# Performance work log

Measured on AMD Instinct MI355X. Metric: run time of the kernel, lower is better.

## Reference

```python
import jax, jax.numpy as jnp
import numpy as np

T, B = 512, 64
IDIM, HDIM = 256, 512
NSTACK, SSZ, SDIM, SDEPTH = 2, 32, 64, 2
NACTS = 3  # push, pop, noop


def setup_inputs() -> dict:
    key = jax.random.key(0)
    ks = jax.random.split(key, 16)
    s = 0.02
    inp = {
        "embs": jax.random.normal(ks[0], (T, B, IDIM), jnp.float32),
        "lens": jax.random.randint(ks[1], (B,), 1, T + 1),
        # emb2hid
        "We": jax.random.normal(ks[2], (HDIM, IDIM), jnp.float32) * s,
        "be": jnp.zeros((HDIM,), jnp.float32),
        # hid2hid
        "Wh": jax.random.normal(ks[3], (HDIM, HDIM), jnp.float32) * s,
        "bh": jnp.zeros((HDIM,), jnp.float32),
        # hid2act
        "Wa": jax.random.normal(ks[4], (NSTACK * NACTS, HDIM), jnp.float32) * s,
        "ba": jnp.zeros((NSTACK * NACTS,), jnp.float32),
        # hid2stack
        "Ws": jax.random.normal(ks[5], (NSTACK * SDIM, HDIM), jnp.float32) * s,
        "bs": jnp.zeros((NSTACK * SDIM,), jnp.float32),
        # stack2hid
        "Wr": jax.random.normal(ks[6], (NSTACK * HDIM, NSTACK * SDIM * SDEPTH), jnp.float32) * s,
        "br": jnp.zeros((NSTACK * HDIM,), jnp.float32),
        # non-trainable stack init bias
        "mem_bias": jax.random.uniform(ks[7], (NSTACK, SDIM), jnp.float32,
                                        -1.0, 1.0) / np.sqrt(NSTACK * SSZ + SDIM),
    }
    return inp


def reference(embs, lens, We, be, Wh, bh, Wa, ba, Ws, bs, Wr, br, mem_bias):
    Tn, Bn, _ = embs.shape
    mem = jnp.broadcast_to(mem_bias[None, :, None, :], (Bn, NSTACK, 1, SDIM))
    stack0 = jnp.broadcast_to(mem_bias[None, :, None, :], (Bn, NSTACK, SSZ, SDIM))
    hid0 = jnp.zeros((Bn, HDIM), embs.dtype)
    res0 = jnp.zeros_like(stack0)

    def step(carry, xs):
        hid, stack, res = carry
        emb, t = xs
        mhid = emb @ We.T + be + hid @ Wh.T + bh
        # read top sdepth cells of each stack
        tops = stack[:, :, :SDEPTH, :].reshape(Bn, -1)
        read = (tops @ Wr.T + br).reshape(Bn, NSTACK, HDIM).sum(axis=1)
        mhid = mhid + read
        # action gating (push/pop/noop) per stack
        act = jax.nn.softmax((hid @ Wa.T + ba).reshape(Bn, NSTACK, NACTS), axis=-1)
        p_push = act[..., 0, None, None]  # [B, nstack, 1, 1]
        p_pop = act[..., 1, None, None]
        p_noop = act[..., 2, None, None]
        push_vals = jnp.tanh((hid @ Ws.T + bs).reshape(Bn, NSTACK, SDIM))
        # push: shift down, write push_vals on top; pop: shift up, mem_bias at bottom
        stack_push = jnp.concatenate([push_vals[:, :, None, :], stack[:, :, :-1, :]], axis=2)
        stack_pop = jnp.concatenate([stack[:, :, 1:, :], mem], axis=2)
        new_stack = p_push * stack_push + p_pop * stack_pop + p_noop * stack
        new_hid = jnp.tanh(mhid)
        new_res = jnp.where((t == lens - 1)[:, None, None, None], new_stack, res)
        return (new_hid, new_stack, new_res), new_hid

    (_, _, stack_res), output = jax.lax.scan(
        step, (hid0, stack0, res0), (embs, jnp.arange(Tn)))
    hid_last = output[lens - 1, jnp.arange(Bn), :][None]  # [1, B, H]
    return output, hid_last, stack_res
```

## Files before the change

### kernel.cpp

```cpp
#include <hip/hip_runtime.h>
#include <hip/hip_bf16.h>
#include <hip/hip_fp16.h>
#include <stdint.h>

constexpr int kT = 512;

constexpr uint32_t WHP_OFF  = 0u;
constexpr uint32_t WRSP_OFF = 524288u;
constexpr uint32_t WSP_OFF  = 786432u;
constexpr uint32_t WEP_OFF  = 917504u;
constexpr uint32_t BIAS_OFF = 1179648u;
constexpr uint32_t X_OFF    = 1181696u;

constexpr uint32_t OUT_HL = 16777216u;
constexpr uint32_t OUT_SR = 16809984u;

static __device__ __forceinline__ float bitsf(uint32_t u) {
  union { uint32_t u; float f; } c; c.u = u; return c.f;
}

typedef _Float16 h2_t __attribute__((ext_vector_type(2)));

static __device__ __forceinline__ float dot2acc(uint32_t w, uint32_t h, float acc) {
#if __has_builtin(__builtin_amdgcn_fdot2)
  return __builtin_amdgcn_fdot2(__builtin_bit_cast(h2_t, w),
                                __builtin_bit_cast(h2_t, h), acc, false);
#else
  h2_t wv = __builtin_bit_cast(h2_t, w), hv = __builtin_bit_cast(h2_t, h);
  return acc + (float)wv.x * (float)hv.x + (float)wv.y * (float)hv.y;
#endif
}

static __device__ __forceinline__ float dot8h(uint4 w, uint4 h, float acc) {
  acc = dot2acc(w.x, h.x, acc);
  acc = dot2acc(w.y, h.y, acc);
  acc = dot2acc(w.z, h.z, acc);
  acc = dot2acc(w.w, h.w, acc);
  return acc;
}

__global__ __launch_bounds__(256) void pack_kernel(
    const float* __restrict__ Wh, const float* __restrict__ Wr,
    const float* __restrict__ Ws, const float* __restrict__ We,
    const float* __restrict__ be, const float* __restrict__ bh,
    const float* __restrict__ br, char* __restrict__ ws)
{
  uint32_t g = blockIdx.x * 256u + threadIdx.x;
  __half* whp  = (__half*)(ws + WHP_OFF);
  __half* wrsp = (__half*)(ws + WRSP_OFF);
  __half* wsp  = (__half*)(ws + WSP_OFF);
  __hip_bfloat16* wep = (__hip_bfloat16*)(ws + WEP_OFF);
  float* bias = (float*)(ws + BIAS_OFF);

  if (g < 262144u) {
    uint32_t e = g & 7u, h = (g >> 3) & 511u, kb = g >> 12;
    whp[g] = __float2half(Wh[h * 512u + kb * 8u + e]);
  }
  if (g < 131072u) {
    uint32_t e = g & 7u, h = (g >> 3) & 511u, jb = g >> 12;
    wrsp[g] = __float2half(Wr[h * 256u + jb * 8u + e] +
                           Wr[(512u + h) * 256u + jb * 8u + e]);
  }
  if (g < 65536u) {
    uint32_t e = g & 7u, o = (g >> 3) & 127u, kb = g >> 10;
    wsp[g] = __float2half(Ws[o * 512u + kb * 8u + e]);
  }
  if (g < 131072u) {
    uint32_t e = g & 7u, h = (g >> 3) & 511u, kb = g >> 12;
    wep[g] = __float2bfloat16(We[h * 256u + kb * 8u + e]);
  }
  if (g < 512u) bias[g] = be[g] + bh[g] + br[g] + br[512u + g];
}

__global__ __launch_bounds__(256) void embed_kernel(
    const float* __restrict__ embs, const char* __restrict__ ws,
    float* __restrict__ out)
{
  __shared__ __align__(16) float embL[16 * 256];
  const uint32_t tid = threadIdx.x;
  const uint32_t r0 = blockIdx.x * 16u;
  #pragma unroll
  for (int i = 0; i < 16; i++) embL[tid + i * 256] = embs[r0 * 256u + tid + i * 256u];
  __syncthreads();

  const uint4* wep = (const uint4*)(ws + WEP_OFF);
  const float* bias = (const float*)(ws + BIAS_OFF);

  for (int hb = 0; hb < 2; hb++) {
    uint32_t h = hb * 256u + tid;
    float acc[16];
    #pragma unroll
    for (int r = 0; r < 16; r++) acc[r] = 0.f;
    for (int kb = 0; kb < 32; kb++) {
      uint4 v = wep[kb * 512u + h];
      float w0 = bitsf(v.x << 16), w1 = bitsf(v.x & 0xffff0000u);
      float w2 = bitsf(v.y << 16), w3 = bitsf(v.y & 0xffff0000u);
      float w4 = bitsf(v.z << 16), w5 = bitsf(v.z & 0xffff0000u);
      float w6 = bitsf(v.w << 16), w7 = bitsf(v.w & 0xffff0000u);
      #pragma unroll
      for (int r = 0; r < 16; r++) {
        const float4* e4 = (const float4*)&embL[r * 256 + kb * 8];
        float4 a = e4[0], c = e4[1];
        acc[r] += w0 * a.x + w1 * a.y + w2 * a.z + w3 * a.w
                + w4 * c.x + w5 * c.y + w6 * c.z + w7 * c.w;
      }
    }
    float bi = bias[h];
    #pragma unroll
    for (int r = 0; r < 16; r++) out[(r0 + r) * 512u + h] = acc[r] + bi;
  }
}

__global__ __launch_bounds__(1024) void rnn_kernel(
    const int* __restrict__ lens, const float* __restrict__ Wa,
    const float* __restrict__ ba, const float* __restrict__ bs,
    const float* __restrict__ memb, char* __restrict__ ws,
    float* __restrict__ out)
{
  __shared__ __align__(16) float stk[2][4096];
  __shared__ __align__(16) __half waH[3072];
  __shared__ __align__(16) __half hH[2][512];
  __shared__ __align__(16) __half tH[2][256];
  __shared__ __align__(16) float pvL[128];
  __shared__ __align__(16) float membL[128];
  __shared__ float bsL[128];
  __shared__ float lgts[8];
  __shared__ float baL[8];

  const uint32_t tid = threadIdx.x;
  const uint32_t wg = blockIdx.x;
  const uint32_t q = wg >> 6;
  const uint32_t b = wg & 63u;
  const int len = lens[b];
  const uint32_t r = tid >> 3, s = tid & 7u;
  const uint32_t h = q * 128u + r;

  const uint4* whp  = (const uint4*)(ws + WHP_OFF);
  const uint4* wrsp = (const uint4*)(ws + WRSP_OFF);
  const uint4* wsp  = (const uint4*)(ws + WSP_OFF);
  uint32_t* X32 = (uint32_t*)(ws + X_OFF);

  uint4 wh[8], wrs[4], wsr[8];
  #pragma unroll
  for (int i = 0; i < 8; i++) wh[i]  = whp[(s * 8u + (uint32_t)i) * 512u + h];
  #pragma unroll
  for (int i = 0; i < 4; i++) wrs[i] = wrsp[(s * 4u + (uint32_t)i) * 512u + h];
  #pragma unroll
  for (int j = 0; j < 8; j++) wsr[j] = wsp[(s * 8u + (uint32_t)j) * 128u + r];

  for (uint32_t i = tid; i < 3072u; i += 1024u) waH[i] = __float2half(Wa[i]);
  if (tid < 128u) { membL[tid] = memb[tid]; bsL[tid] = bs[tid]; }
  if (tid < 64u)  ((uint4*)hH[0])[tid] = uint4{0u, 0u, 0u, 0u};
  if (tid < 256u) {
    uint32_t jb = tid >> 3, e = tid & 7u, n = tid >> 7, d = tid & 63u;
    uint32_t pt = ((jb & 3u) << 3) | (jb >> 2);
    ((__half*)tH[0])[pt * 8u + e] = __float2half(memb[n * 64u + d]);
  }
  if (tid < 8u) baL[tid] = (tid < 6u) ? ba[tid] : 0.f;
  __syncthreads();
  {
    uint32_t c = tid * 4u, n = c >> 11, d = c & 63u;
    *(float4*)&stk[0][c] = *(const float4*)&membL[n * 64u + d];
  }
  float eCur = (s == 0) ? out[b * 512u + h] : 0.f;
  __syncthreads();

  for (int t = 0; t < kT; t++) {
    const int cur = t & 1, nxt = cur ^ 1;
    const bool lastT = (t == len - 1);
    const uint4* hc = (const uint4*)hH[cur];
    const uint4* tc = (const uint4*)tH[cur];

    float eNext = (s == 0 && t < kT - 1)
                ? out[((uint32_t)(t + 1) * 64u + b) * 512u + h] : 0.f;

    float acc = 0.f;
    #pragma unroll
    for (int i = 0; i < 8; i++) acc = dot8h(wh[i], hc[(uint32_t)i * 8u + s], acc);
    #pragma unroll
    for (int i = 0; i < 4; i++) acc = dot8h(wrs[i], tc[(uint32_t)i * 8u + s], acc);
    acc += __shfl_xor(acc, 1, 64);
    acc += __shfl_xor(acc, 2, 64);
    acc += __shfl_xor(acc, 4, 64);
    if (s == 0) {
      float v = tanhf(acc + eCur);
      out[((uint32_t)t * 64u + b) * 512u + h] = v;
      if (lastT) out[OUT_HL + b * 512u + h] = v;
      __half vh = __float2half(v);
      uint32_t pay = ((uint32_t)(t + 1) << 16) | (uint32_t)__half_as_ushort(vh);
      __hip_atomic_store(&X32[(((uint32_t)cur * 64u + b) * 4u + q) * 128u + r], pay,
                         __ATOMIC_RELAXED, __HIP_MEMORY_SCOPE_AGENT);
      uint32_t kb = h >> 3, e = h & 7u;
      uint32_t ph = ((kb & 7u) << 3) | (kb >> 3);
      ((__half*)hH[nxt])[ph * 8u + e] = vh;
    }
    eCur = eNext;

    float wa2 = 0.f;
    #pragma unroll
    for (int j = 0; j < 8; j++) wa2 = dot8h(wsr[j], hc[((uint32_t)j << 3) | s], wa2);
    wa2 += __shfl_xor(wa2, 1, 64);
    wa2 += __shfl_xor(wa2, 2, 64);
    wa2 += __shfl_xor(wa2, 4, 64);
    if (s == 0) pvL[r] = tanhf(wa2 + bsL[r]);

    if (tid < 384u) {
      uint32_t o = tid >> 6, kb = tid & 63u;
      uint32_t ph = ((kb & 7u) << 3) | (kb >> 3);
      float la = dot8h(((const uint4*)waH)[o * 64u + kb], hc[ph], 0.f);
      #pragma unroll
      for (int off = 1; off <= 32; off <<= 1) la += __shfl_xor(la, off, 64);
      if (kb == 0) lgts[o] = la + baL[o];
    }
    __syncthreads();

    {
      uint32_t c = tid * 4u;
      uint32_t n = c >> 11, sd = (tid >> 4) & 31u, d = c & 63u;
      float l0 = lgts[n * 3u], l1 = lgts[n * 3u + 1u], l2 = lgts[n * 3u + 2u];
      float m = fmaxf(l0, fmaxf(l1, l2));
      float e0 = __expf(l0 - m), e1 = __expf(l1 - m), e2 = __expf(l2 - m);
      float inv = 1.f / (e0 + e1 + e2);
      float p0 = e0 * inv, p1 = e1 * inv, p2 = e2 * inv;
      float4 scur = *(const float4*)&stk[cur][c];
      float4 sp = (sd == 0) ? *(const float4*)&pvL[n * 64u + d]
                            : *(const float4*)&stk[cur][c - 64u];
      float4 so = (sd == 31u) ? *(const float4*)&membL[n * 64u + d]
                              : *(const float4*)&stk[cur][c + 64u];
      float4 nv;
      nv.x = p0 * sp.x + p1 * so.x + p2 * scur.x;
      nv.y = p0 * sp.y + p1 * so.y + p2 * scur.y;
      nv.z = p0 * sp.z + p1 * so.z + p2 * scur.z;
      nv.w = p0 * sp.w + p1 * so.w + p2 * scur.w;
      *(float4*)&stk[nxt][c] = nv;
      if (sd < 2u) {
        uint32_t f = n * 128u + sd * 64u + d;
        uint32_t jb = f >> 3, e = f & 7u;
        uint32_t pt = ((jb & 3u) << 3) | (jb >> 2);
        uint32_t lo = ((uint32_t)__half_as_ushort(__float2half(nv.y)) << 16) |
                      __half_as_ushort(__float2half(nv.x));
        uint32_t hi = ((uint32_t)__half_as_ushort(__float2half(nv.w)) << 16) |
                      __half_as_ushort(__float2half(nv.z));
        *(uint2*)((__half*)tH[nxt] + pt * 8u + e) = uint2{lo, hi};
      }
      if (lastT && q == 0u) *(float4*)&out[OUT_SR + b * 4096u + c] = nv;
    }

    if (t < kT - 1 && tid < 384u) {
      uint32_t j = tid >> 7;
      uint32_t jj = j + (j >= q ? 1u : 0u);
      uint32_t k = tid & 127u;
      uint32_t* src = &X32[(((uint32_t)cur * 64u + b) * 4u + jj) * 128u + k];
      const uint32_t want = (uint32_t)(t + 1) << 16;
      uint32_t x = __hip_atomic_load(src, __ATOMIC_RELAXED, __HIP_MEMORY_SCOPE_AGENT);
      uint32_t g = 0;
      while ((x & 0xffff0000u) != want) {
        x = __hip_atomic_load(src, __ATOMIC_RELAXED, __HIP_MEMORY_SCOPE_AGENT);
        if (++g > (1u << 24)) break;
      }
      uint32_t idx = jj * 128u + k, kb = idx >> 3, e = idx & 7u;
      uint32_t ph = ((kb & 7u) << 3) | (kb >> 3);
      ((__half*)hH[nxt])[ph * 8u + e] = __ushort_as_half((unsigned short)(x & 0xffffu));
    }
    __syncthreads();
  }
}

extern "C" void kernel_launch(void* const* d_in, const int* in_sizes, int n_in,
                              void* d_out, int out_size, void* d_ws, size_t ws_size,
                              hipStream_t stream) {
  const float* embs = (const float*)d_in[0];
  const int*   lens = (const int*)d_in[1];
  const float* We   = (const float*)d_in[2];
  const float* be   = (const float*)d_in[3];
  const float* Wh   = (const float*)d_in[4];
  const float* bh   = (const float*)d_in[5];
  const float* Wa   = (const float*)d_in[6];
  const float* ba   = (const float*)d_in[7];
  const float* Ws   = (const float*)d_in[8];
  const float* bs   = (const float*)d_in[9];
  const float* Wr   = (const float*)d_in[10];
  const float* br   = (const float*)d_in[11];
  const float* memb = (const float*)d_in[12];
  float* out = (float*)d_out;
  char* ws = (char*)d_ws;

  pack_kernel<<<1024, 256, 0, stream>>>(Wh, Wr, Ws, We, be, bh, br, ws);
  embed_kernel<<<2048, 256, 0, stream>>>(embs, ws, out);
  rnn_kernel<<<256, 1024, 0, stream>>>(lens, Wa, ba, bs, memb, ws, out);
}
```

Baseline: 1.281 ms.

## Process two batch rows per workgroup with doubled per-thread weight registers

The recurrent kernel now handles two batch elements per workgroup, with 512 threads instead of 1024 and 128 blocks instead of 256. Each thread holds twice as many weight registers (4-way K split instead of 8-way), so each weight is reused across two sequences. The layouts of the hidden and top-of-stack shared buffers change to match. The aim is to halve total weight register and load traffic and shorten the shuffle reductions. The cost is higher register pressure (forced live with asm keep-alives), fewer workgroups, and more serial work per step on the latency-bound recurrence.

```diff
diff --git a/kernel.cpp b/kernel.cpp
--- a/kernel.cpp
+++ b/kernel.cpp
@@ -38,6 +38,8 @@
   acc = dot2acc(w.w, h.w, acc);
   return acc;
 }
+
+#define KEEP4(v) asm volatile("" : "+v"((v).x), "+v"((v).y), "+v"((v).z), "+v"((v).w))
 
 __global__ __launch_bounds__(256) void pack_kernel(
     const float* __restrict__ Wh, const float* __restrict__ Wr,
@@ -111,28 +113,29 @@
   }
 }
 
-__global__ __launch_bounds__(1024) void rnn_kernel(
+__global__ __launch_bounds__(512, 2) void rnn_kernel(
     const int* __restrict__ lens, const float* __restrict__ Wa,
     const float* __restrict__ ba, const float* __restrict__ bs,
     const float* __restrict__ memb, char* __restrict__ ws,
     float* __restrict__ out)
 {
-  __shared__ __align__(16) float stk[2][4096];
+  __shared__ __align__(16) float stk[2][2][4096];
   __shared__ __align__(16) __half waH[3072];
-  __shared__ __align__(16) __half hH[2][512];
-  __shared__ __align__(16) __half tH[2][256];
-  __shared__ __align__(16) float pvL[128];
+  __shared__ __align__(16) __half hH[2][2][512];
+  __shared__ __align__(16) __half tH[2][2][256];
+  __shared__ __align__(16) float pvL[2][128];
   __shared__ __align__(16) float membL[128];
   __shared__ float bsL[128];
-  __shared__ float lgts[8];
+  __shared__ float lgts[2][8];
   __shared__ float baL[8];
 
   const uint32_t tid = threadIdx.x;
   const uint32_t wg = blockIdx.x;
-  const uint32_t q = wg >> 6;
-  const uint32_t b = wg & 63u;
-  const int len = lens[b];
-  const uint32_t r = tid >> 3, s = tid & 7u;
+  const uint32_t q = wg >> 5;
+  const uint32_t p = wg & 31u;
+  const uint32_t b0 = 2u * p, b1 = 2u * p + 1u;
+  const int len0 = lens[b0], len1 = lens[b1];
+  const uint32_t r = tid >> 2, s = tid & 3u;
   const uint32_t h = q * 128u + r;
 
   const uint4* whp  = (const uint4*)(ws + WHP_OFF);
@@ -140,127 +143,161 @@
   const uint4* wsp  = (const uint4*)(ws + WSP_OFF);
   uint32_t* X32 = (uint32_t*)(ws + X_OFF);
 
-  uint4 wh[8], wrs[4], wsr[8];
-  #pragma unroll
-  for (int i = 0; i < 8; i++) wh[i]  = whp[(s * 8u + (uint32_t)i) * 512u + h];
-  #pragma unroll
-  for (int i = 0; i < 4; i++) wrs[i] = wrsp[(s * 4u + (uint32_t)i) * 512u + h];
-  #pragma unroll
-  for (int j = 0; j < 8; j++) wsr[j] = wsp[(s * 8u + (uint32_t)j) * 128u + r];
-
-  for (uint32_t i = tid; i < 3072u; i += 1024u) waH[i] = __float2half(Wa[i]);
-  if (tid < 128u) { membL[tid] = memb[tid]; bsL[tid] = bs[tid]; }
-  if (tid < 64u)  ((uint4*)hH[0])[tid] = uint4{0u, 0u, 0u, 0u};
-  if (tid < 256u) {
-    uint32_t jb = tid >> 3, e = tid & 7u, n = tid >> 7, d = tid & 63u;
-    uint32_t pt = ((jb & 3u) << 3) | (jb >> 2);
-    ((__half*)tH[0])[pt * 8u + e] = __float2half(memb[n * 64u + d]);
+  uint4 wh[16], wrs[8], wsr[16];
+  #pragma unroll
+  for (int i = 0; i < 16; i++) wh[i]  = whp[(s * 16u + (uint32_t)i) * 512u + h];
+  #pragma unroll
+  for (int i = 0; i < 8; i++)  wrs[i] = wrsp[(s * 8u + (uint32_t)i) * 512u + h];
+  #pragma unroll
+  for (int i = 0; i < 16; i++) wsr[i] = wsp[(s * 16u + (uint32_t)i) * 128u + r];
+  #pragma unroll
+  for (int i = 0; i < 16; i++) KEEP4(wh[i]);
+  #pragma unroll
+  for (int i = 0; i < 8; i++)  KEEP4(wrs[i]);
+  #pragma unroll
+  for (int i = 0; i < 16; i++) KEEP4(wsr[i]);
+
+  for (uint32_t i = tid; i < 3072u; i += 512u) waH[i] = __float2half(Wa[i]);
+  if (tid < 128u) {
+    membL[tid] = memb[tid]; bsL[tid] = bs[tid];
+    uint32_t u = tid >> 6, sl = tid & 63u;
+    ((uint4*)hH[u][0])[sl] = uint4{0u, 0u, 0u, 0u};
+  }
+  {
+    uint32_t u = tid >> 8, f = tid & 255u;
+    uint32_t jb = f >> 3, e = f & 7u, n = f >> 7, d = f & 63u;
+    uint32_t pt = ((jb & 7u) << 2) | (jb >> 3);
+    ((__half*)tH[u][0])[pt * 8u + e] = __float2half(memb[n * 64u + d]);
   }
   if (tid < 8u) baL[tid] = (tid < 6u) ? ba[tid] : 0.f;
   __syncthreads();
-  {
-    uint32_t c = tid * 4u, n = c >> 11, d = c & 63u;
-    *(float4*)&stk[0][c] = *(const float4*)&membL[n * 64u + d];
-  }
-  float eCur = (s == 0) ? out[b * 512u + h] : 0.f;
+  #pragma unroll
+  for (int u = 0; u < 2; u++) {
+    #pragma unroll
+    for (int hv = 0; hv < 2; hv++) {
+      uint32_t c = tid * 8u + (uint32_t)hv * 4u;
+      uint32_t n = c >> 11, d = c & 63u;
+      *(float4*)&stk[u][0][c] = *(const float4*)&membL[n * 64u + d];
+    }
+  }
+  float eCur0 = (s == 0) ? out[b0 * 512u + h] : 0.f;
+  float eCur1 = (s == 0) ? out[b1 * 512u + h] : 0.f;
   __syncthreads();
 
   for (int t = 0; t < kT; t++) {
     const int cur = t & 1, nxt = cur ^ 1;
-    const bool lastT = (t == len - 1);
-    const uint4* hc = (const uint4*)hH[cur];
-    const uint4* tc = (const uint4*)tH[cur];
-
-    float eNext = (s == 0 && t < kT - 1)
-                ? out[((uint32_t)(t + 1) * 64u + b) * 512u + h] : 0.f;
-
-    float acc = 0.f;
-    #pragma unroll
-    for (int i = 0; i < 8; i++) acc = dot8h(wh[i], hc[(uint32_t)i * 8u + s], acc);
-    #pragma unroll
-    for (int i = 0; i < 4; i++) acc = dot8h(wrs[i], tc[(uint32_t)i * 8u + s], acc);
-    acc += __shfl_xor(acc, 1, 64);
-    acc += __shfl_xor(acc, 2, 64);
-    acc += __shfl_xor(acc, 4, 64);
-    if (s == 0) {
-      float v = tanhf(acc + eCur);
-      out[((uint32_t)t * 64u + b) * 512u + h] = v;
-      if (lastT) out[OUT_HL + b * 512u + h] = v;
-      __half vh = __float2half(v);
-      uint32_t pay = ((uint32_t)(t + 1) << 16) | (uint32_t)__half_as_ushort(vh);
-      __hip_atomic_store(&X32[(((uint32_t)cur * 64u + b) * 4u + q) * 128u + r], pay,
-                         __ATOMIC_RELAXED, __HIP_MEMORY_SCOPE_AGENT);
-      uint32_t kb = h >> 3, e = h & 7u;
-      uint32_t ph = ((kb & 7u) << 3) | (kb >> 3);
-      ((__half*)hH[nxt])[ph * 8u + e] = vh;
-    }
-    eCur = eNext;
-
-    float wa2 = 0.f;
-    #pragma unroll
-    for (int j = 0; j < 8; j++) wa2 = dot8h(wsr[j], hc[((uint32_t)j << 3) | s], wa2);
-    wa2 += __shfl_xor(wa2, 1, 64);
-    wa2 += __shfl_xor(wa2, 2, 64);
-    wa2 += __shfl_xor(wa2, 4, 64);
-    if (s == 0) pvL[r] = tanhf(wa2 + bsL[r]);
-
-    if (tid < 384u) {
-      uint32_t o = tid >> 6, kb = tid & 63u;
-      uint32_t ph = ((kb & 7u) << 3) | (kb >> 3);
-      float la = dot8h(((const uint4*)waH)[o * 64u + kb], hc[ph], 0.f);
-      #pragma unroll
-      for (int off = 1; off <= 32; off <<= 1) la += __shfl_xor(la, off, 64);
-      if (kb == 0) lgts[o] = la + baL[o];
-    }
+    float eN0 = 0.f, eN1 = 0.f;
+    if (s == 0 && t < kT - 1) {
+      eN0 = out[((uint32_t)(t + 1) * 64u + b0) * 512u + h];
+      eN1 = out[((uint32_t)(t + 1) * 64u + b1) * 512u + h];
+    }
+
+    #pragma unroll
+    for (int u = 0; u < 2; u++) {
+      const uint32_t bu = u ? b1 : b0;
+      const float eC = u ? eCur1 : eCur0;
+      const int lenU = u ? len1 : len0;
+      const uint4* hc = (const uint4*)hH[u][cur];
+      const uint4* tc = (const uint4*)tH[u][cur];
+
+      float acc = 0.f;
+      #pragma unroll
+      for (int i = 0; i < 16; i++) acc = dot8h(wh[i], hc[(uint32_t)i * 4u + s], acc);
+      #pragma unroll
+      for (int i = 0; i < 8; i++)  acc = dot8h(wrs[i], tc[(uint32_t)i * 4u + s], acc);
+      acc += __shfl_xor(acc, 1, 64);
+      acc += __shfl_xor(acc, 2, 64);
+      if (s == 0) {
+        float v = tanhf(acc + eC);
+        out[((uint32_t)t * 64u + bu) * 512u + h] = v;
+        if (t == lenU - 1) out[OUT_HL + bu * 512u + h] = v;
+        __half vh = __float2half(v);
+        uint32_t pay = ((uint32_t)(t + 1) << 16) | (uint32_t)__half_as_ushort(vh);
+        __hip_atomic_store(&X32[(((uint32_t)cur * 64u + bu) * 4u + q) * 128u + r], pay,
+                           __ATOMIC_RELAXED, __HIP_MEMORY_SCOPE_AGENT);
+        uint32_t kb = h >> 3, e = h & 7u;
+        uint32_t ph = ((kb & 15u) << 2) | (kb >> 4);
+        ((__half*)hH[u][nxt])[ph * 8u + e] = vh;
+      }
+      float wa2 = 0.f;
+      #pragma unroll
+      for (int i = 0; i < 16; i++) wa2 = dot8h(wsr[i], hc[(uint32_t)i * 4u + s], wa2);
+      wa2 += __shfl_xor(wa2, 1, 64);
+      wa2 += __shfl_xor(wa2, 2, 64);
+      if (s == 0) pvL[u][r] = tanhf(wa2 + bsL[r]);
+      if (tid < 384u) {
+        uint32_t o = tid >> 6, kb = tid & 63u;
+        uint32_t ph = ((kb & 15u) << 2) | (kb >> 4);
+        float la = dot8h(((const uint4*)waH)[o * 64u + kb], hc[ph], 0.f);
+        #pragma unroll
+        for (int off = 1; off <= 32; off <<= 1) la += __shfl_xor(la, off, 64);
+        if (kb == 0) lgts[u][o] = la + baL[o];
+      }
+    }
+    eCur0 = eN0; eCur1 = eN1;
     __syncthreads();
 
-    {
-      uint32_t c = tid * 4u;
-      uint32_t n = c >> 11, sd = (tid >> 4) & 31u, d = c & 63u;
-      float l0 = lgts[n * 3u], l1 = lgts[n * 3u + 1u], l2 = lgts[n * 3u + 2u];
+    #pragma unroll
+    for (int u = 0; u < 2; u++) {
+      const uint32_t bu = u ? b1 : b0;
+      const int lenU = u ? len1 : len0;
+      const bool lastT = (t == lenU - 1);
+      uint32_t c0 = tid * 8u;
+      uint32_t n = c0 >> 11, sd = (c0 >> 6) & 31u;
+      float l0 = lgts[u][n * 3u], l1 = lgts[u][n * 3u + 1u], l2 = lgts[u][n * 3u + 2u];
       float m = fmaxf(l0, fmaxf(l1, l2));
       float e0 = __expf(l0 - m), e1 = __expf(l1 - m), e2 = __expf(l2 - m);
       float inv = 1.f / (e0 + e1 + e2);
       float p0 = e0 * inv, p1 = e1 * inv, p2 = e2 * inv;
-      float4 scur = *(const float4*)&stk[cur][c];
-      float4 sp = (sd == 0) ? *(const float4*)&pvL[n * 64u + d]
-                            : *(const float4*)&stk[cur][c - 64u];
-      float4 so = (sd == 31u) ? *(const float4*)&membL[n * 64u + d]
-                              : *(const float4*)&stk[cur][c + 64u];
-      float4 nv;
-      nv.x = p0 * sp.x + p1 * so.x + p2 * scur.x;
-      nv.y = p0 * sp.y + p1 * so.y + p2 * scur.y;
-      nv.z = p0 * sp.z + p1 * so.z + p2 * scur.z;
-      nv.w = p0 * sp.w + p1 * so.w + p2 * scur.w;
-      *(float4*)&stk[nxt][c] = nv;
-      if (sd < 2u) {
-        uint32_t f = n * 128u + sd * 64u + d;
-        uint32_t jb = f >> 3, e = f & 7u;
-        uint32_t pt = ((jb & 3u) << 3) | (jb >> 2);
-        uint32_t lo = ((uint32_t)__half_as_ushort(__float2half(nv.y)) << 16) |
-                      __half_as_ushort(__float2half(nv.x));
-        uint32_t hi = ((uint32_t)__half_as_ushort(__float2half(nv.w)) << 16) |
-                      __half_as_ushort(__float2half(nv.z));
-        *(uint2*)((__half*)tH[nxt] + pt * 8u + e) = uint2{lo, hi};
-      }
-      if (lastT && q == 0u) *(float4*)&out[OUT_SR + b * 4096u + c] = nv;
+      #pragma unroll
+      for (int hv = 0; hv < 2; hv++) {
+        uint32_t c = c0 + (uint32_t)hv * 4u;
+        uint32_t d = c & 63u;
+        float4 scur = *(const float4*)&stk[u][cur][c];
+        float4 sp = (sd == 0) ? *(const float4*)&pvL[u][n * 64u + d]
+                              : *(const float4*)&stk[u][cur][c - 64u];
+        float4 so = (sd == 31u) ? *(const float4*)&membL[n * 64u + d]
+                                : *(const float4*)&stk[u][cur][c + 64u];
+        float4 nv;
+        nv.x = p0 * sp.x + p1 * so.x + p2 * scur.x;
+        nv.y = p0 * sp.y + p1 * so.y + p2 * scur.y;
+        nv.z = p0 * sp.z + p1 * so.z + p2 * scur.z;
+        nv.w = p0 * sp.w + p1 * so.w + p2 * scur.w;
+        *(float4*)&stk[u][nxt][c] = nv;
+        if (sd < 2u) {
+          uint32_t f = n * 128u + sd * 64u + d;
+          uint32_t jb = f >> 3, e = f & 7u;
+          uint32_t pt = ((jb & 7u) << 2) | (jb >> 3);
+          uint32_t lo = ((uint32_t)__half_as_ushort(__float2half(nv.y)) << 16) |
+                        __half_as_ushort(__float2half(nv.x));
+          uint32_t hi = ((uint32_t)__half_as_ushort(__float2half(nv.w)) << 16) |
+                        __half_as_ushort(__float2half(nv.z));
+          *(uint2*)((__half*)tH[u][nxt] + pt * 8u + e) = uint2{lo, hi};
+        }
+        if (lastT && q == 0u) *(float4*)&out[OUT_SR + bu * 4096u + c] = nv;
+      }
     }
 
     if (t < kT - 1 && tid < 384u) {
-      uint32_t j = tid >> 7;
-      uint32_t jj = j + (j >= q ? 1u : 0u);
-      uint32_t k = tid & 127u;
-      uint32_t* src = &X32[(((uint32_t)cur * 64u + b) * 4u + jj) * 128u + k];
-      const uint32_t want = (uint32_t)(t + 1) << 16;
-      uint32_t x = __hip_atomic_load(src, __ATOMIC_RELAXED, __HIP_MEMORY_SCOPE_AGENT);
-      uint32_t g = 0;
-      while ((x & 0xffff0000u) != want) {
-        x = __hip_atomic_load(src, __ATOMIC_RELAXED, __HIP_MEMORY_SCOPE_AGENT);
-        if (++g > (1u << 24)) break;
-      }
-      uint32_t idx = jj * 128u + k, kb = idx >> 3, e = idx & 7u;
-      uint32_t ph = ((kb & 7u) << 3) | (kb >> 3);
-      ((__half*)hH[nxt])[ph * 8u + e] = __ushort_as_half((unsigned short)(x & 0xffffu));
+      #pragma unroll
+      for (int u = 0; u < 2; u++) {
+        const uint32_t bu = u ? b1 : b0;
+        uint32_t j = tid >> 7;
+        uint32_t jj = j + (j >= q ? 1u : 0u);
+        uint32_t k = tid & 127u;
+        uint32_t* src = &X32[(((uint32_t)cur * 64u + bu) * 4u + jj) * 128u + k];
+        const uint32_t want = (uint32_t)(t + 1) << 16;
+        uint32_t x = __hip_atomic_load(src, __ATOMIC_RELAXED, __HIP_MEMORY_SCOPE_AGENT);
+        uint32_t g = 0;
+        while ((x & 0xffff0000u) != want) {
+          x = __hip_atomic_load(src, __ATOMIC_RELAXED, __HIP_MEMORY_SCOPE_AGENT);
+          if (++g > (1u << 24)) break;
+        }
+        uint32_t idx = jj * 128u + k, kb = idx >> 3, e = idx & 7u;
+        uint32_t ph = ((kb & 15u) << 2) | (kb >> 4);
+        ((__half*)hH[u][nxt])[ph * 8u + e] =
+            __ushort_as_half((unsigned short)(x & 0xffffu));
+      }
     }
     __syncthreads();
   }
@@ -287,5 +324,5 @@
 
   pack_kernel<<<1024, 256, 0, stream>>>(Wh, Wr, Ws, We, be, bh, br, ws);
   embed_kernel<<<2048, 256, 0, stream>>>(embs, ws, out);
-  rnn_kernel<<<256, 1024, 0, stream>>>(lens, Wa, ba, bs, memb, ws, out);
-}
+  rnn_kernel<<<128, 512, 0, stream>>>(lens, Wa, ba, bs, memb, ws, out);
+}
```

New measurement: 2.443 ms. 1.91x slower.
